# Kernel tuning notes

Measured on AMD Instinct MI355X. Metric: run time of the kernel, lower is better.

## Reference

```python
import jax, jax.numpy as jnp
import numpy as np

BSZ, SEQ, ENC, TMAX = 32, 4096, 512, 64

def setup_inputs() -> dict:
    key = jax.random.key(0)
    k1, k2, k3, k4, k5 = jax.random.split(key, 5)
    encoder_output = jax.random.normal(k1, (BSZ, SEQ, ENC), dtype=jnp.float32)
    his_turn_end_ids = jnp.sort(jax.random.randint(k2, (BSZ, TMAX), 0, SEQ), axis=-1)
    # original: turn_lengths[i] = len(his_turn_end_ids[i]); ensure >= 2 so loss path is taken
    turn_lengths = 2 + jax.random.randint(k3, (BSZ,), 0, TMAX - 1)
    W = jax.random.normal(k4, (2, 2 * ENC), dtype=jnp.float32) * 0.02  # nn.Linear(enc_dim*2, 2).weight
    b = jax.random.normal(k5, (2,), dtype=jnp.float32) * 0.02
    return {"encoder_output": encoder_output, "his_turn_end_ids": his_turn_end_ids,
            "turn_lengths": turn_lengths, "W": W, "b": b}

def reference(encoder_output, his_turn_end_ids, turn_lengths, W, b):
    bsz, tmax = his_turn_end_ids.shape
    enc = encoder_output.shape[-1]
    # ragged gather of turn-end states: [bsz, tmax, enc]
    his = jnp.take_along_axis(encoder_output, his_turn_end_ids[:, :, None], axis=1)
    # concat([left, right]) @ W.T == left @ Wl.T + right @ Wr.T  (avoids [b,T,T,2*enc] tensor)
    Wl, Wr = W[:, :enc], W[:, enc:]
    left = jnp.einsum('btd,od->bto', his, Wl)   # [bsz, tmax, 2]
    right = jnp.einsum('btd,od->bto', his, Wr)  # [bsz, tmax, 2]
    logits = left[:, :, None, :] + right[:, None, :, :] + b  # [bsz, j, k, 2]
    jj = jnp.arange(tmax)[None, :, None]
    kk = jnp.arange(tmax)[None, None, :]
    valid = (kk < jj) & (jj < turn_lengths[:, None, None])  # pairs (j,k) with k<j, j<len_i
    labels = (kk == jj - 1)  # 1 iff k == j-1
    logp = jax.nn.log_softmax(logits, axis=-1)
    ce = -jnp.where(labels, logp[..., 1], logp[..., 0])
    cnt = jnp.maximum(jnp.sum(valid), 1)
    loss = jnp.sum(jnp.where(valid, ce, 0.0)) / cnt.astype(ce.dtype)
    return loss
```

## Files before the change

kernel.cpp:

```cpp
#include <hip/hip_runtime.h>
#include <math.h>

#define BSZ 32
#define SEQ 4096
#define ENCD 512
#define TMAX 64

__device__ __forceinline__ float dot4(float4 a, float4 b) {
    return a.x * b.x + a.y * b.y + a.z * b.z + a.w * b.w;
}

__global__ __launch_bounds__(64) void lr_kernel(
    const float* __restrict__ enc, const int* __restrict__ ids,
    const float* __restrict__ W, float4* __restrict__ lr) {
    int bt = blockIdx.x;
    int b = bt >> 6;
    int lane = threadIdx.x;
    int id = ids[bt];
    const float4* x4 = (const float4*)(enc + ((size_t)b * SEQ + (size_t)id) * ENCD) + lane * 2;
    const float4* wl0 = (const float4*)(W) + lane * 2;
    const float4* wr0 = (const float4*)(W + ENCD) + lane * 2;
    const float4* wl1 = (const float4*)(W + 2 * ENCD) + lane * 2;
    const float4* wr1 = (const float4*)(W + 3 * ENCD) + lane * 2;

    float4 xa = x4[0], xb = x4[1];
    float s0 = dot4(xa, wl0[0]) + dot4(xb, wl0[1]);
    float s1 = dot4(xa, wl1[0]) + dot4(xb, wl1[1]);
    float s2 = dot4(xa, wr0[0]) + dot4(xb, wr0[1]);
    float s3 = dot4(xa, wr1[0]) + dot4(xb, wr1[1]);

#pragma unroll
    for (int off = 32; off; off >>= 1) {
        s0 += __shfl_down(s0, off);
        s1 += __shfl_down(s1, off);
        s2 += __shfl_down(s2, off);
        s3 += __shfl_down(s3, off);
    }
    if (lane == 0) lr[bt] = make_float4(s0, s1, s2, s3);
}

__global__ __launch_bounds__(256) void pair_kernel(
    const float4* __restrict__ lr, const int* __restrict__ tlen,
    const float* __restrict__ bias, float* __restrict__ partial) {
    int b = blockIdx.x;
    int tid = threadIdx.x;
    __shared__ float4 slr[TMAX];
    __shared__ float ssum[4], scnt[4];
    if (tid < TMAX) slr[tid] = lr[b * TMAX + tid];
    __syncthreads();

    int T = tlen[b];
    float b0 = bias[0], b1 = bias[1];
    float sum = 0.f, cnt = 0.f;
    for (int idx = tid; idx < TMAX * TMAX; idx += 256) {
        int j = idx >> 6, k = idx & 63;
        if (k < j && j < T) {
            float4 Lj = slr[j];
            float4 Rk = slr[k];
            float l0 = Lj.x + Rk.z + b0;
            float l1 = Lj.y + Rk.w + b1;
            float m = fmaxf(l0, l1);
            float lse = m + logf(expf(l0 - m) + expf(l1 - m));
            float lp = (k == j - 1) ? (l1 - lse) : (l0 - lse);
            sum -= lp;
            cnt += 1.f;
        }
    }
#pragma unroll
    for (int off = 32; off; off >>= 1) {
        sum += __shfl_down(sum, off);
        cnt += __shfl_down(cnt, off);
    }
    int wave = tid >> 6;
    if ((tid & 63) == 0) { ssum[wave] = sum; scnt[wave] = cnt; }
    __syncthreads();
    if (tid == 0) {
        float S = ssum[0] + ssum[1] + ssum[2] + ssum[3];
        float C = scnt[0] + scnt[1] + scnt[2] + scnt[3];
        partial[b * 2] = S;
        partial[b * 2 + 1] = C;
    }
}

__global__ __launch_bounds__(64) void final_kernel(
    const float* __restrict__ partial, float* __restrict__ out) {
    int lane = threadIdx.x;
    float s = 0.f, c = 0.f;
    if (lane < BSZ) { s = partial[lane * 2]; c = partial[lane * 2 + 1]; }
#pragma unroll
    for (int off = 32; off; off >>= 1) {
        s += __shfl_down(s, off);
        c += __shfl_down(c, off);
    }
    if (lane == 0) out[0] = s / fmaxf(c, 1.f);
}

extern "C" void kernel_launch(void* const* d_in, const int* in_sizes, int n_in,
                              void* d_out, int out_size, void* d_ws, size_t ws_size,
                              hipStream_t stream) {
    const float* enc  = (const float*)d_in[0];
    const int*   ids  = (const int*)d_in[1];
    const int*   tlen = (const int*)d_in[2];
    const float* W    = (const float*)d_in[3];
    const float* bias = (const float*)d_in[4];
    float* out = (float*)d_out;

    float4* lr      = (float4*)d_ws;
    float*  partial = (float*)((char*)d_ws + BSZ * TMAX * sizeof(float4));

    lr_kernel<<<BSZ * TMAX, 64, 0, stream>>>(enc, ids, W, lr);
    pair_kernel<<<BSZ, 256, 0, stream>>>(lr, tlen, bias, partial);
    final_kernel<<<1, 64, 0, stream>>>(partial, out);
}
```

Before: 304.0 us.

## Fuse gather-projection kernel into per-batch pair-loss kernel

Merges the row-gather/projection kernel into the pair-loss kernel so each batch block gathers its 64 turn-end rows, projects them into shared memory, and then computes the pairwise loss. This removes one kernel launch and the workspace round trip for the projected values. The cost is much lower parallelism for the gather phase, since only 32 blocks do work that was previously spread over 2048 blocks. Each wave now handles 16 rows with 4 loads in flight.

After: 309.2 us. Within noise of the previous version (+1.7%).

```diff
diff --git a/kernel.cpp b/kernel.cpp
--- a/kernel.cpp
+++ b/kernel.cpp
@@ -10,43 +10,55 @@
     return a.x * b.x + a.y * b.y + a.z * b.z + a.w * b.w;
 }
 
-__global__ __launch_bounds__(64) void lr_kernel(
+__global__ __launch_bounds__(256) void fused_kernel(
     const float* __restrict__ enc, const int* __restrict__ ids,
-    const float* __restrict__ W, float4* __restrict__ lr) {
-    int bt = blockIdx.x;
-    int b = bt >> 6;
-    int lane = threadIdx.x;
-    int id = ids[bt];
-    const float4* x4 = (const float4*)(enc + ((size_t)b * SEQ + (size_t)id) * ENCD) + lane * 2;
-    const float4* wl0 = (const float4*)(W) + lane * 2;
-    const float4* wr0 = (const float4*)(W + ENCD) + lane * 2;
-    const float4* wl1 = (const float4*)(W + 2 * ENCD) + lane * 2;
-    const float4* wr1 = (const float4*)(W + 3 * ENCD) + lane * 2;
-
-    float4 xa = x4[0], xb = x4[1];
-    float s0 = dot4(xa, wl0[0]) + dot4(xb, wl0[1]);
-    float s1 = dot4(xa, wl1[0]) + dot4(xb, wl1[1]);
-    float s2 = dot4(xa, wr0[0]) + dot4(xb, wr0[1]);
-    float s3 = dot4(xa, wr1[0]) + dot4(xb, wr1[1]);
-
-#pragma unroll
-    for (int off = 32; off; off >>= 1) {
-        s0 += __shfl_down(s0, off);
-        s1 += __shfl_down(s1, off);
-        s2 += __shfl_down(s2, off);
-        s3 += __shfl_down(s3, off);
-    }
-    if (lane == 0) lr[bt] = make_float4(s0, s1, s2, s3);
-}
-
-__global__ __launch_bounds__(256) void pair_kernel(
-    const float4* __restrict__ lr, const int* __restrict__ tlen,
+    const int* __restrict__ tlen, const float* __restrict__ W,
     const float* __restrict__ bias, float* __restrict__ partial) {
     int b = blockIdx.x;
     int tid = threadIdx.x;
+    int lane = tid & 63;
+    int wv = tid >> 6;
+
+    __shared__ int sids[TMAX];
     __shared__ float4 slr[TMAX];
     __shared__ float ssum[4], scnt[4];
-    if (tid < TMAX) slr[tid] = lr[b * TMAX + tid];
+
+    if (tid < TMAX) sids[tid] = ids[b * TMAX + tid];
+    __syncthreads();
+
+    const float4* W4 = (const float4*)W;
+    int l2 = lane * 2;
+    float4 wl0a = W4[l2],       wl0b = W4[l2 + 1];
+    float4 wr0a = W4[128 + l2], wr0b = W4[128 + l2 + 1];
+    float4 wl1a = W4[256 + l2], wl1b = W4[256 + l2 + 1];
+    float4 wr1a = W4[384 + l2], wr1b = W4[384 + l2 + 1];
+
+    for (int t0 = wv * 16; t0 < wv * 16 + 16; t0 += 4) {
+        float4 xa[4], xb[4];
+#pragma unroll
+        for (int r = 0; r < 4; r++) {
+            int id = sids[t0 + r];
+            const float4* x4 =
+                (const float4*)(enc + ((size_t)b * SEQ + (size_t)id) * ENCD) + l2;
+            xa[r] = x4[0];
+            xb[r] = x4[1];
+        }
+#pragma unroll
+        for (int r = 0; r < 4; r++) {
+            float s0 = dot4(xa[r], wl0a) + dot4(xb[r], wl0b);
+            float s1 = dot4(xa[r], wl1a) + dot4(xb[r], wl1b);
+            float s2 = dot4(xa[r], wr0a) + dot4(xb[r], wr0b);
+            float s3 = dot4(xa[r], wr1a) + dot4(xb[r], wr1b);
+#pragma unroll
+            for (int off = 32; off; off >>= 1) {
+                s0 += __shfl_down(s0, off);
+                s1 += __shfl_down(s1, off);
+                s2 += __shfl_down(s2, off);
+                s3 += __shfl_down(s3, off);
+            }
+            if (lane == 0) slr[t0 + r] = make_float4(s0, s1, s2, s3);
+        }
+    }
     __syncthreads();
 
     int T = tlen[b];
@@ -71,8 +83,7 @@
         sum += __shfl_down(sum, off);
         cnt += __shfl_down(cnt, off);
     }
-    int wave = tid >> 6;
-    if ((tid & 63) == 0) { ssum[wave] = sum; scnt[wave] = cnt; }
+    if (lane == 0) { ssum[wv] = sum; scnt[wv] = cnt; }
     __syncthreads();
     if (tid == 0) {
         float S = ssum[0] + ssum[1] + ssum[2] + ssum[3];
@@ -105,10 +116,8 @@
     const float* bias = (const float*)d_in[4];
     float* out = (float*)d_out;
 
-    float4* lr      = (float4*)d_ws;
-    float*  partial = (float*)((char*)d_ws + BSZ * TMAX * sizeof(float4));
+    float* partial = (float*)d_ws;
 
-    lr_kernel<<<BSZ * TMAX, 64, 0, stream>>>(enc, ids, W, lr);
-    pair_kernel<<<BSZ, 256, 0, stream>>>(lr, tlen, bias, partial);
+    fused_kernel<<<BSZ, 256, 0, stream>>>(enc, ids, tlen, W, bias, partial);
     final_kernel<<<1, 64, 0, stream>>>(partial, out);
 }
```
